# Kernel optimization log

Measured on AMD Instinct MI355X. Metric: run time of the kernel, lower is better.

Reference implementation:

```python
import jax, jax.numpy as jnp
import numpy as np

B, CIN, H, W = 4, 272, 32, 32
D, NHEAD, DFF, E, TOPK, NDEC = 256, 8, 1024, 8, 2, 2
HW = H * W


def _sine_pos():
    npf = D // 2
    ye = jnp.cumsum(jnp.ones((H, W), jnp.float32), 0)
    xe = jnp.cumsum(jnp.ones((H, W), jnp.float32), 1)
    eps, scale = 1e-6, 2.0 * np.pi
    ye = ye / (ye[-1:, :] + eps) * scale
    xe = xe / (xe[:, -1:] + eps) * scale
    t = jnp.arange(npf, dtype=jnp.float32)
    dim_t = 10000.0 ** (2.0 * jnp.floor(t / 2.0) / npf)
    px = xe[:, :, None] / dim_t
    py = ye[:, :, None] / dim_t
    px = jnp.stack((jnp.sin(px[:, :, 0::2]), jnp.cos(px[:, :, 1::2])), axis=3).reshape(H, W, npf)
    py = jnp.stack((jnp.sin(py[:, :, 0::2]), jnp.cos(py[:, :, 1::2])), axis=3).reshape(H, W, npf)
    return jnp.concatenate((py, px), axis=2).reshape(HW, D)


def _ln(v, g, b):
    m = v.mean(-1, keepdims=True)
    var = ((v - m) ** 2).mean(-1, keepdims=True)
    return (v - m) / jnp.sqrt(var + 1e-5) * g + b


def _mha(q_in, k_in, v_in, Wqkv, bqkv, Wo, bo):
    # seq-first [S,B,D], torch nn.MultiheadAttention math (dropout off)
    S = q_in.shape[0]; T = k_in.shape[0]; dh = D // NHEAD
    Wq, Wk, Wv = jnp.split(Wqkv, 3, 0)
    bq, bk, bv = jnp.split(bqkv, 3)
    q = (q_in @ Wq.T + bq).reshape(S, B, NHEAD, dh)
    k = (k_in @ Wk.T + bk).reshape(T, B, NHEAD, dh)
    v = (v_in @ Wv.T + bv).reshape(T, B, NHEAD, dh)
    attn = jax.nn.softmax(jnp.einsum('sbhd,tbhd->bhst', q, k) / np.sqrt(dh), axis=-1)
    o = jnp.einsum('bhst,tbhd->sbhd', attn, v).reshape(S, B, D)
    return o @ Wo.T + bo


def _moe(xt, Wg, bg, W1, b1, W2, b2):
    # FMoETransformerMLP with NaiveGate: top-k gate, per-expert 2-layer MLP, weighted combine
    S = xt.shape[0]
    xf = xt.reshape(-1, D)
    N = xf.shape[0]
    logits = xf @ Wg.T + bg                              # [N, E]
    topv, topi = jax.lax.top_k(logits, TOPK)             # [N, k]
    score = jax.nn.softmax(topv, axis=-1)                # softmax over selected logits
    comb = jnp.zeros((N, E), xf.dtype).at[jnp.arange(N)[:, None], topi].add(score)
    h = jax.nn.relu(jnp.einsum('nd,edh->neh', xf, W1) + b1)   # [N, E, DFF]
    y = jnp.einsum('neh,ehd->ned', h, W2) + b2                # [N, E, D]
    out = jnp.einsum('ne,ned->nd', comb, y)
    return out.reshape(S, B, D)


def setup_inputs() -> dict:
    key = jax.random.key(0)
    ks = iter(jax.random.split(key, 32))
    g = lambda shp, s=0.02: s * jax.random.normal(next(ks), shp, jnp.float32)
    inp = {
        'x': jax.random.normal(next(ks), (B, CIN, H, W), jnp.float32),
        'Wi': g((D, CIN)), 'bi': jnp.zeros((D,), jnp.float32),
        'learned_embed': g((HW, D), 1.0),
        'Wqkv_s': g((3 * D, D)), 'bqkv_s': jnp.zeros((3 * D,), jnp.float32),
        'Wo_s': g((D, D)), 'bo_s': jnp.zeros((D,), jnp.float32),
        'Wqkv_c': g((3 * D, D)), 'bqkv_c': jnp.zeros((3 * D,), jnp.float32),
        'Wo_c': g((D, D)), 'bo_c': jnp.zeros((D,), jnp.float32),
        'ln_g': jnp.ones((4 * NDEC, D), jnp.float32), 'ln_b': jnp.zeros((4 * NDEC, D), jnp.float32),
        'gate_w1': g((E, D)), 'gate_b1': jnp.zeros((E,), jnp.float32),
        'W1a': g((E, D, DFF)), 'b1a': jnp.zeros((E, DFF), jnp.float32),
        'W2a': g((E, DFF, D)), 'b2a': jnp.zeros((E, D), jnp.float32),
        'gate_w2': g((E, D)), 'gate_b2': jnp.zeros((E,), jnp.float32),
        'W1b': g((E, D, DFF)), 'b1b': jnp.zeros((E, DFF), jnp.float32),
        'W2b': g((E, DFF, D)), 'b2b': jnp.zeros((E, D), jnp.float32),
        'Wout': g((CIN, D)), 'bout': jnp.zeros((CIN,), jnp.float32),
    }
    return inp


def reference(x, Wi, bi, learned_embed, Wqkv_s, bqkv_s, Wo_s, bo_s,
              Wqkv_c, bqkv_c, Wo_c, bo_c, ln_g, ln_b,
              gate_w1, gate_b1, W1a, b1a, W2a, b2a,
              gate_w2, gate_b2, W1b, b1b, W2b, b2b, Wout, bout):
    tokens = x.transpose(2, 3, 0, 1).reshape(HW, B, CIN)   # 'b c h w -> (h w) b c'
    src = tokens @ Wi.T + bi                               # input_proj
    pos = _sine_pos()[:, None, :]                          # [HW,1,D] broadcast over batch
    enc = src
    dec = src
    for i in range(NDEC):
        tgt = jnp.broadcast_to(learned_embed[:, None, :], (HW, B, D))
        t2 = _mha(tgt + pos, enc + pos, enc, Wqkv_s, bqkv_s, Wo_s, bo_s)
        tgt = _ln(tgt + t2, ln_g[4 * i], ln_b[4 * i])
        t2 = _mha(tgt + pos, dec + pos, dec, Wqkv_c, bqkv_c, Wo_c, bo_c)
        tgt = _ln(tgt + t2, ln_g[4 * i + 1], ln_b[4 * i + 1])
        od = tgt + _moe(tgt, gate_w1, gate_b1, W1a, b1a, W2a, b2a)   # post-lnorm: residual only
        od = _ln(od, ln_g[4 * i + 2], ln_b[4 * i + 2])
        od = od + _moe(od, gate_w2, gate_b2, W1b, b1b, W2b, b2b)
        dec = _ln(od, ln_g[4 * i + 3], ln_b[4 * i + 3])
    rec = dec @ Wout.T + bout                              # output_proj, [HW,B,CIN]
    feature_rec = rec.reshape(H, W, B, CIN).transpose(2, 3, 0, 1)
    return feature_rec
```

## Files before the change

### kernel.cpp

```cpp
#include <hip/hip_runtime.h>

#define NHW 1024
#define NB 4
#define DM 256
#define NTOK 4096
#define NCIN 272
#define NDFF 1024

typedef unsigned short u16;
typedef unsigned int u32;
typedef __attribute__((ext_vector_type(8))) short s16x8;
typedef __attribute__((ext_vector_type(4))) float f32x4;

static const int GEMM_SMEM32 = (32+32+64+64)*56*2;
static const int GEMM_SMEM64 = (32+32+64+64)*72*2;

__device__ __forceinline__ float4 ld4(const float* p){ return *(const float4*)p; }
__device__ __forceinline__ void st4(float* p, float4 v){ *(float4*)p = v; }

__device__ __forceinline__ void splitf(float x, u16& h, u16& l){
  u32 u = __float_as_uint(x);
  u32 hu = (u + (0x7FFFu + ((u >> 16) & 1u))) >> 16;
  h = (u16)hu;
  float hf = __uint_as_float(hu << 16);
  float r = x - hf;
  u32 v = __float_as_uint(r);
  v += 0x7FFFu + ((v >> 16) & 1u);
  l = (u16)(v >> 16);
}

__device__ __forceinline__ u32 packf(float x){
  u16 h,l; splitf(x,h,l);
  return (u32)h | ((u32)l << 16);
}

__global__ void pos_kernel(float* __restrict__ pos){
  int s = blockIdx.x, d = threadIdx.x;
  int row = s >> 5, col = s & 31;
  float base = (d < 128) ? (float)(row + 1) : (float)(col + 1);
  float val = base / (32.0f + 1e-6f) * 6.2831853071795864f;
  int dd = (d < 128) ? d : d - 128;
  int mf = dd >> 1;
  float f = powf(10000.0f, (float)mf * (1.0f/64.0f));
  float a = val / f;
  pos[s*DM + d] = (dd & 1) ? cosf(a) : sinf(a);
}

__global__ void tin_kernel(const float* __restrict__ x, float* __restrict__ tok){
  int idx = blockIdx.x*256 + threadIdx.x;
  if (idx >= NTOK*NCIN) return;
  int c = idx % NCIN;
  int n = idx / NCIN;
  int s = n >> 2, b = n & 3;
  tok[idx] = x[((long)(b*NCIN + c))*NHW + s];
}
__global__ void tout_kernel(const float* __restrict__ rec, float* __restrict__ out){
  int idx = blockIdx.x*256 + threadIdx.x;
  if (idx >= NTOK*NCIN) return;
  int s = idx & (NHW-1);
  int bc = idx >> 10;
  int b = bc / NCIN, c = bc % NCIN;
  out[idx] = rec[((long)(s*NB + b))*NCIN + c];
}

__global__ __launch_bounds__(256) void tconv_kernel(const float* __restrict__ in,
    u16* __restrict__ oh, u16* __restrict__ ol, int K, int N){
  __shared__ float tile[32][33];
  long base = (long)blockIdx.z * (long)K * (long)N;
  int k0 = blockIdx.y*32, n0 = blockIdx.x*32;
  int tx = threadIdx.x & 31, ty = threadIdx.x >> 5;
  #pragma unroll
  for (int i=0;i<32;i+=8)
    tile[ty+i][tx] = in[base + (long)(k0+ty+i)*N + n0+tx];
  __syncthreads();
  #pragma unroll
  for (int i=0;i<32;i+=8){
    float v = tile[tx][ty+i];
    u16 h,l; splitf(v,h,l);
    long o = base + (long)(n0+ty+i)*K + k0+tx;
    oh[o]=h; ol[o]=l;
  }
}

__global__ void wsplit_kernel(const float* __restrict__ in, u16* __restrict__ oh,
    u16* __restrict__ ol, int n){
  int i = blockIdx.x*256 + threadIdx.x;
  if (i < n){ u16 h,l; splitf(in[i],h,l); oh[i]=h; ol[i]=l; }
}

template<bool GROUPED, bool INDIRECT, int ASRC, bool RELU, int CDST, int BK>
__device__ __forceinline__ void sgemm_body(
    const void* __restrict__ Av, int lda,
    const float* __restrict__ pos,
    const u16* __restrict__ Bhp, const u16* __restrict__ Blp, int ldb,
    const float* __restrict__ bias,
    void* __restrict__ Cv, int ldc,
    int M, int N, int K,
    const int* __restrict__ map,
    const int* __restrict__ cnt,
    const int* __restrict__ offs,
    const int* __restrict__ jmap,
    const float* __restrict__ sflat,
    long strideB, int strideBias, int e)
{
  constexpr int BM = 32;
  constexpr int NSEG = BK/32;
  constexpr int SW = (BK==32) ? 56 : 72;
  int rows = GROUPED ? cnt[e] : M;
  int bn = blockIdx.x, bm = blockIdx.y;
  if (bm*BM >= rows) return;
  int row0 = GROUPED ? offs[e] : 0;
  const float* Af = (const float*)Av;
  const u32*   Ap = (const u32*)Av;
  if (GROUPED){ Bhp += (long)e*strideB; Blp += (long)e*strideB; }
  const float* biasp = bias ? (GROUPED ? bias + (long)e*strideBias : bias) : nullptr;

  extern __shared__ u16 smem[];
  u16* Ah = smem;
  u16* Al = Ah + BM*SW;
  u16* Bh = Al + BM*SW;
  u16* Bl = Bh + 64*SW;

  int tid = threadIdx.x;
  int w = tid >> 6, ln = tid & 63;
  int wm = w >> 1, wn = w & 1;
  int lr = ln & 15, lh = ln >> 4;
  int srow = tid >> 2, sseg = tid & 3;

  int bgrow = bn*64 + srow;
  bool bok = bgrow < N;
  int agrow = bm*BM + srow;
  bool aok = (tid < BM*4) && (agrow < rows);
  long arow = 0;
  if (aok) arow = INDIRECT ? (long)map[row0 + agrow] : (long)(row0 + agrow);

  const f32x4 z4 = {0.f,0.f,0.f,0.f};
  f32x4 acc0 = z4, acc1 = z4;
  const s16x8 z8 = {0,0,0,0,0,0,0,0};

  s16x8 rBh[NSEG], rBl[NSEG];
  uint4 rA0[NSEG], rA1[NSEG];
  float4 rP0[NSEG], rP1[NSEG];
  float rinv[NSEG];

  auto load_stage = [&](int k0){
    #pragma unroll
    for (int s=0; s<NSEG; s++){
      int kk = k0 + s*32 + sseg*8;
      bool kok = kk < K;
      rBh[s] = z8; rBl[s] = z8;
      if (bok && kok){
        rBh[s] = *(const s16x8*)&Bhp[(long)bgrow*ldb + kk];
        rBl[s] = *(const s16x8*)&Blp[(long)bgrow*ldb + kk];
      }
      if (tid < BM*4){
        rA0[s] = make_uint4(0,0,0,0); rA1[s] = make_uint4(0,0,0,0);
        if (ASRC==2 || ASRC==3 || ASRC==5){
          rP0[s] = make_float4(0.f,0.f,0.f,0.f); rP1[s] = rP0[s]; rinv[s] = 0.f;
        }
        if (aok && kok){
          if (ASRC == 1){
            rA0[s] = *(const uint4*)&Ap[arow*lda + kk];
            rA1[s] = *(const uint4*)&Ap[arow*lda + kk + 4];
          } else if (ASRC == 5){
            long aoff = arow*(long)lda + kk;
            rA0[s] = *(const uint4*)&Af[aoff];
            rA1[s] = *(const uint4*)&Af[aoff + 4];
            rP0[s] = ld4(&Af[(long)NTOK*DM + aoff]);
            rP1[s] = ld4(&Af[(long)NTOK*DM + aoff + 4]);
            int h = kk >> 5;
            float l0 = pos[arow*8 + h];
            float l1 = pos[65536 + arow*8 + h];
            rinv[s] = 1.f / (l0 + l1);
          } else {
            long aoff = (ASRC==3 ? (long)(arow>>2) : arow)*lda + kk;
            rA0[s] = *(const uint4*)&Af[aoff];
            rA1[s] = *(const uint4*)&Af[aoff + 4];
            if (ASRC==2 || ASRC==3){
              long poff = (long)(arow>>2)*DM + kk;
              rP0[s] = ld4(&pos[poff]);
              rP1[s] = ld4(&pos[poff + 4]);
            }
          }
        }
      }
    }
  };

  auto write_stage = [&](){
    #pragma unroll
    for (int s=0; s<NSEG; s++){
      *(s16x8*)&Bh[srow*SW + s*32 + sseg*8] = rBh[s];
      *(s16x8*)&Bl[srow*SW + s*32 + sseg*8] = rBl[s];
      if (tid < BM*4){
        s16x8 hv, lv;
        if (ASRC == 1){
          u32 ws[8] = {rA0[s].x,rA0[s].y,rA0[s].z,rA0[s].w,rA1[s].x,rA1[s].y,rA1[s].z,rA1[s].w};
          #pragma unroll
          for (int t=0;t<8;t++){ hv[t]=(short)(ws[t]&0xFFFFu); lv[t]=(short)(ws[t]>>16); }
        } else {
          float xs[8] = {__uint_as_float(rA0[s].x),__uint_as_float(rA0[s].y),
                         __uint_as_float(rA0[s].z),__uint_as_float(rA0[s].w),
                         __uint_as_float(rA1[s].x),__uint_as_float(rA1[s].y),
                         __uint_as_float(rA1[s].z),__uint_as_float(rA1[s].w)};
          if (ASRC==2 || ASRC==3){
            xs[0]+=rP0[s].x; xs[1]+=rP0[s].y; xs[2]+=rP0[s].z; xs[3]+=rP0[s].w;
            xs[4]+=rP1[s].x; xs[5]+=rP1[s].y; xs[6]+=rP1[s].z; xs[7]+=rP1[s].w;
          }
          if (ASRC==5){
            float iv = rinv[s];
            xs[0]=(xs[0]+rP0[s].x)*iv; xs[1]=(xs[1]+rP0[s].y)*iv;
            xs[2]=(xs[2]+rP0[s].z)*iv; xs[3]=(xs[3]+rP0[s].w)*iv;
            xs[4]=(xs[4]+rP1[s].x)*iv; xs[5]=(xs[5]+rP1[s].y)*iv;
            xs[6]=(xs[6]+rP1[s].z)*iv; xs[7]=(xs[7]+rP1[s].w)*iv;
          }
          #pragma unroll
          for (int t=0;t<8;t++){ u16 hh,ll; splitf(xs[t],hh,ll); hv[t]=(short)hh; lv[t]=(short)ll; }
        }
        *(s16x8*)&Ah[srow*SW + s*32 + sseg*8] = hv;
        *(s16x8*)&Al[srow*SW + s*32 + sseg*8] = lv;
      }
    }
  };

  load_stage(0);
  for (int k0 = 0; k0 < K; k0 += BK){
    write_stage();
    __syncthreads();
    if (k0 + BK < K) load_stage(k0 + BK);
    #pragma unroll
    for (int s=0; s<NSEG; s++){
      int co = s*32 + lh*8;
      s16x8 a0h = *(const s16x8*)&Ah[(wm*16 + lr)*SW + co];
      s16x8 a0l = *(const s16x8*)&Al[(wm*16 + lr)*SW + co];
      s16x8 b0h = *(const s16x8*)&Bh[(wn*32      + lr)*SW + co];
      s16x8 b1h = *(const s16x8*)&Bh[(wn*32 + 16 + lr)*SW + co];
      s16x8 b0l = *(const s16x8*)&Bl[(wn*32      + lr)*SW + co];
      s16x8 b1l = *(const s16x8*)&Bl[(wn*32 + 16 + lr)*SW + co];
      acc0 = __builtin_amdgcn_mfma_f32_16x16x32_bf16(a0h, b0h, acc0, 0,0,0);
      acc1 = __builtin_amdgcn_mfma_f32_16x16x32_bf16(a0h, b1h, acc1, 0,0,0);
      acc0 = __builtin_amdgcn_mfma_f32_16x16x32_bf16(a0h, b0l, acc0, 0,0,0);
      acc1 = __builtin_amdgcn_mfma_f32_16x16x32_bf16(a0h, b1l, acc1, 0,0,0);
      acc0 = __builtin_amdgcn_mfma_f32_16x16x32_bf16(a0l, b0h, acc0, 0,0,0);
      acc1 = __builtin_amdgcn_mfma_f32_16x16x32_bf16(a0l, b1h, acc1, 0,0,0);
    }
    __syncthreads();
  }

  int c0 = bn*64 + wn*32 + lr;
  int c1 = c0 + 16;
  float bv0 = (biasp && c0 < N) ? biasp[c0] : 0.f;
  float bv1 = (biasp && c1 < N) ? biasp[c1] : 0.f;
  int rbase = bm*BM + wm*16 + lh*4;
  auto stc = [&](int gr, int gc, float vv){
    if (gr < rows && gc < N){
      float t = RELU ? fmaxf(vv, 0.f) : vv;
      if (CDST == 1){
        ((u32*)Cv)[(long)(row0+gr)*ldc + gc] = packf(t);
      } else if (CDST == 2){
        int ts = jmap[row0+gr];
        ((float*)Cv)[(long)ts*ldc + gc] = t * sflat[ts];
      } else {
        ((float*)Cv)[(long)(row0+gr)*ldc + gc] = t;
      }
    }
  };
  #pragma unroll
  for (int r = 0; r < 4; r++){
    stc(rbase + r, c0, acc0[r] + bv0);
    stc(rbase + r, c1, acc1[r] + bv1);
  }
}

__global__ __launch_bounds__(256) void gemm_in(const float* A, const u16* Bh_, const u16* Bl_,
    const float* bias, float* C){
  sgemm_body<false,false,0,false,0,32>(A, NCIN, nullptr, Bh_, Bl_, NCIN, bias, C, DM,
      NTOK, DM, NCIN, nullptr, nullptr, nullptr, nullptr, nullptr, 0, 0, 0);
}

__global__ __launch_bounds__(256) void gemm_out_k(const float* A, const u16* Bh_, const u16* Bl_,
    const float* bias, float* C){
  sgemm_body<false,false,0,false,0,32>(A, DM, nullptr, Bh_, Bl_, DM, bias, C, NCIN,
      NTOK, NCIN, DM, nullptr, nullptr, nullptr, nullptr, nullptr, 0, 0, 0);
}

__global__ __launch_bounds__(256) void gemm_wos(const float* OpB, const float* lB,
    const u16* Bh_, const u16* Bl_, const float* bias, float* C){
  sgemm_body<false,false,5,false,0,32>(OpB, DM, lB, Bh_, Bl_, DM, bias, C, DM,
      NTOK, DM, DM, nullptr, nullptr, nullptr, nullptr, nullptr, 0, 0, 0);
}

__global__ __launch_bounds__(256) void gemm_woc(const float* OpB, const float* lB,
    const u16* Bh_, const u16* Bl_, const float* bias, float* C){
  sgemm_body<false,false,5,false,0,32>(OpB, DM, lB, Bh_, Bl_, DM, bias, C, DM,
      NTOK, DM, DM, nullptr, nullptr, nullptr, nullptr, nullptr, 0, 0, 0);
}

template<int MQ, int MK>
__device__ __forceinline__ void qkv_body(const float* Aq, const float* Ak, const float* Avv,
    const float* pos, const u16* Bwh, const u16* Bwl, const float* bias,
    u32* Cq, u32* Ck, u32* Cvv){
  int z = blockIdx.z;
  const float* A = z==0 ? Aq : (z==1 ? Ak : Avv);
  u32* C = z==0 ? Cq : (z==1 ? Ck : Cvv);
  const u16* Bph = Bwh + (long)z*256*DM;
  const u16* Bpl = Bwl + (long)z*256*DM;
  const float* bp = bias + z*256;
  int mode = z==0 ? MQ : (z==1 ? MK : 0);
  if (mode == 3)
    sgemm_body<false,false,3,false,1,32>(A, DM, pos, Bph, Bpl, DM, bp, C, DM,
        NTOK, DM, DM, nullptr, nullptr, nullptr, nullptr, nullptr, 0, 0, 0);
  else if (mode == 2)
    sgemm_body<false,false,2,false,1,32>(A, DM, pos, Bph, Bpl, DM, bp, C, DM,
        NTOK, DM, DM, nullptr, nullptr, nullptr, nullptr, nullptr, 0, 0, 0);
  else
    sgemm_body<false,false,0,false,1,32>(A, DM, pos, Bph, Bpl, DM, bp, C, DM,
        NTOK, DM, DM, nullptr, nullptr, nullptr, nullptr, nullptr, 0, 0, 0);
}

__global__ __launch_bounds__(256) void gemm_qkv_s(const float* Aq, const float* Ak,
    const float* Avv, const float* pos, const u16* Bwh, const u16* Bwl, const float* bias,
    u32* Cq, u32* Ck, u32* Cvv){
  qkv_body<3,2>(Aq, Ak, Avv, pos, Bwh, Bwl, bias, Cq, Ck, Cvv);
}
__global__ __launch_bounds__(256) void gemm_qkv_c(const float* Aq, const float* Ak,
    const float* Avv, const float* pos, const u16* Bwh, const u16* Bwl, const float* bias,
    u32* Cq, u32* Ck, u32* Cvv){
  qkv_body<2,2>(Aq, Ak, Avv, pos, Bwh, Bwl, bias, Cq, Ck, Cvv);
}

__global__ __launch_bounds__(256) void gemm_m1(const float* A, const u16* Bh_, const u16* Bl_,
    const float* bias, u32* C, const int* map, const int* cnt, const int* offs){
  sgemm_body<true,true,0,true,1,32>(A, DM, nullptr, Bh_, Bl_, DM, bias, C, NDFF,
      0, NDFF, DM, map, cnt, offs, nullptr, nullptr, 262144L, NDFF, blockIdx.z);
}

__global__ __launch_bounds__(256) void gemm_m2(const u32* A, const u16* Bh_, const u16* Bl_,
    const float* bias, float* C, const int* cnt, const int* offs,
    const int* jmap, const float* sflat){
  sgemm_body<true,false,1,false,2,64>(A, NDFF, nullptr, Bh_, Bl_, NDFF, bias, C, DM,
      0, DM, NDFF, nullptr, cnt, offs, jmap, sflat, 262144L, DM, blockIdx.z);
}

__global__ __launch_bounds__(256) void attn_mfma(const u32* __restrict__ Q,
    const u32* __restrict__ Kb, const u32* __restrict__ Vb,
    float* __restrict__ OpBase, float* __restrict__ lBase)
{
  __shared__ u16 Kh[64*40], Kl[64*40];
  __shared__ u16 Vh[32*72], Vl[32*72];
  __shared__ u16 Ph[4][16*72], Pl[4][16*72];

  int qt = blockIdx.x, bh = blockIdx.y, z = blockIdx.z;
  int b = bh >> 3, h = bh & 7;
  int tid = threadIdx.x;
  int wv = tid >> 6, ln = tid & 63;
  int lr = ln & 15, lh = ln >> 4;
  const float scale = 0.17677669529663687f;
  int kt0 = z*8, kt1 = z*8 + 8;
  float* Op   = OpBase + (long)z*NTOK*DM;
  float* lArr = lBase + (long)z*65536;

  s16x8 qh, ql;
  {
    long qrow = ((long)((qt*64 + wv*16 + lr)*NB + b))*DM + h*32 + lh*8;
    uint4 p0 = *(const uint4*)&Q[qrow];
    uint4 p1 = *(const uint4*)&Q[qrow + 4];
    u32 ws[8] = {p0.x,p0.y,p0.z,p0.w,p1.x,p1.y,p1.z,p1.w};
    #pragma unroll
    for (int t=0;t<8;t++){ qh[t]=(short)(ws[t]&0xFFFFu); ql[t]=(short)(ws[t]>>16); }
  }

  int skey = tid >> 2, soct = tid & 3;
  int vkey0 = tid >> 3,        vd0 = (tid & 7) << 2;
  int vkey1 = (tid + 256) >> 3, vd1 = ((tid + 256) & 7) << 2;

  uint4 rK0, rK1, rV0, rV1;

  auto load_kv = [&](int kt){
    long gk = ((long)((kt*64 + skey)*NB + b))*DM + h*32 + soct*8;
    rK0 = *(const uint4*)&Kb[gk];
    rK1 = *(const uint4*)&Kb[gk + 4];
    rV0 = *(const uint4*)&Vb[((long)((kt*64 + vkey0)*NB + b))*DM + h*32 + vd0];
    rV1 = *(const uint4*)&Vb[((long)((kt*64 + vkey1)*NB + b))*DM + h*32 + vd1];
  };

  auto write_kv = [&](){
    u32 ws[8] = {rK0.x,rK0.y,rK0.z,rK0.w,rK1.x,rK1.y,rK1.z,rK1.w};
    s16x8 hv, lv;
    #pragma unroll
    for (int t=0;t<8;t++){ hv[t]=(short)(ws[t]&0xFFFFu); lv[t]=(short)(ws[t]>>16); }
    *(s16x8*)&Kh[skey*40 + soct*8] = hv;
    *(s16x8*)&Kl[skey*40 + soct*8] = lv;
    u32 v0[4] = {rV0.x,rV0.y,rV0.z,rV0.w};
    u32 v1[4] = {rV1.x,rV1.y,rV1.z,rV1.w};
    #pragma unroll
    for (int t=0;t<4;t++){
      Vh[(vd0+t)*72 + vkey0] = (u16)(v0[t]&0xFFFFu);
      Vl[(vd0+t)*72 + vkey0] = (u16)(v0[t]>>16);
      Vh[(vd1+t)*72 + vkey1] = (u16)(v1[t]&0xFFFFu);
      Vl[(vd1+t)*72 + vkey1] = (u16)(v1[t]>>16);
    }
  };

  const f32x4 z4 = {0.f,0.f,0.f,0.f};
  f32x4 oacc0 = z4, oacc1 = z4;
  float lp[4] = {0.f,0.f,0.f,0.f};

  load_kv(kt0);
  for (int kt = kt0; kt < kt1; kt++){
    write_kv();
    __syncthreads();
    if (kt + 1 < kt1) load_kv(kt + 1);

    #pragma unroll
    for (int s16t=0; s16t<4; s16t++){
      s16x8 kbh = *(const s16x8*)&Kh[(s16t*16 + lr)*40 + lh*8];
      s16x8 kbl = *(const s16x8*)&Kl[(s16t*16 + lr)*40 + lh*8];
      f32x4 a = z4;
      a = __builtin_amdgcn_mfma_f32_16x16x32_bf16(qh, kbh, a, 0,0,0);
      a = __builtin_amdgcn_mfma_f32_16x16x32_bf16(qh, kbl, a, 0,0,0);
      a = __builtin_amdgcn_mfma_f32_16x16x32_bf16(ql, kbh, a, 0,0,0);
      #pragma unroll
      for (int r=0;r<4;r++){
        float p = __expf(a[r]*scale);
        lp[r] += p;
        u16 hh,ll; splitf(p,hh,ll);
        int off = (lh*4 + r)*72 + s16t*16 + lr;
        Ph[wv][off] = hh;
        Pl[wv][off] = ll;
      }
    }
    #pragma unroll
    for (int ks=0; ks<2; ks++){
      s16x8 pah = *(const s16x8*)&Ph[wv][lr*72 + ks*32 + lh*8];
      s16x8 pal = *(const s16x8*)&Pl[wv][lr*72 + ks*32 + lh*8];
      s16x8 vh0 = *(const s16x8*)&Vh[lr*72      + ks*32 + lh*8];
      s16x8 vl0 = *(const s16x8*)&Vl[lr*72      + ks*32 + lh*8];
      s16x8 vh1 = *(const s16x8*)&Vh[(16+lr)*72 + ks*32 + lh*8];
      s16x8 vl1 = *(const s16x8*)&Vl[(16+lr)*72 + ks*32 + lh*8];
      oacc0 = __builtin_amdgcn_mfma_f32_16x16x32_bf16(pah, vh0, oacc0, 0,0,0);
      oacc0 = __builtin_amdgcn_mfma_f32_16x16x32_bf16(pah, vl0, oacc0, 0,0,0);
      oacc0 = __builtin_amdgcn_mfma_f32_16x16x32_bf16(pal, vh0, oacc0, 0,0,0);
      oacc1 = __builtin_amdgcn_mfma_f32_16x16x32_bf16(pah, vh1, oacc1, 0,0,0);
      oacc1 = __builtin_amdgcn_mfma_f32_16x16x32_bf16(pah, vl1, oacc1, 0,0,0);
      oacc1 = __builtin_amdgcn_mfma_f32_16x16x32_bf16(pal, vh1, oacc1, 0,0,0);
    }
    __syncthreads();
  }
  #pragma unroll
  for (int mask=1; mask<=8; mask<<=1){
    #pragma unroll
    for (int r=0;r<4;r++) lp[r] += __shfl_xor(lp[r], mask);
  }
  #pragma unroll
  for (int r=0;r<4;r++){
    int q = qt*64 + wv*16 + lh*4 + r;
    long n = (long)q*NB + b;
    long orow = n*DM + h*32;
    Op[orow + lr]      = oacc0[r];
    Op[orow + 16 + lr] = oacc1[r];
    if (lr == 0) lArr[n*8 + h] = lp[r];
  }
}

__device__ __forceinline__ float wave_sum(float v){
  #pragma unroll
  for (int m=1; m<64; m<<=1) v += __shfl_xor(v, m);
  return v;
}

__device__ __forceinline__ float4 ln_finish(float4 a, const float* g, const float* beta, int lane){
  float sum = wave_sum(a.x+a.y+a.z+a.w);
  float sq  = wave_sum(a.x*a.x + a.y*a.y + a.z*a.z + a.w*a.w);
  float mean = sum * (1.f/DM);
  float var  = sq * (1.f/DM) - mean*mean;
  float inv = 1.0f / sqrtf(var + 1e-5f);
  float4 gg = ld4(&g[lane*4]);
  float4 bb = ld4(&beta[lane*4]);
  float4 ov;
  ov.x = (a.x-mean)*inv*gg.x + bb.x;
  ov.y = (a.y-mean)*inv*gg.y + bb.y;
  ov.z = (a.z-mean)*inv*gg.z + bb.z;
  ov.w = (a.w-mean)*inv*gg.w + bb.w;
  return ov;
}

__device__ __forceinline__ void gate_from_regs(float4 ov, int row, int lane,
    const float* GW, const float* GB, float* scores, int* topi){
  float lg[8];
  #pragma unroll
  for (int e=0; e<8; e++){
    float4 wv = ld4(&GW[e*DM + lane*4]);
    lg[e] = ov.x*wv.x + ov.y*wv.y + ov.z*wv.z + ov.w*wv.w;
  }
  #pragma unroll
  for (int mask=1; mask<64; mask<<=1){
    #pragma unroll
    for (int e=0; e<8; e++) lg[e] += __shfl_xor(lg[e], mask);
  }
  #pragma unroll
  for (int e=0; e<8; e++) lg[e] += GB[e];
  int i0 = 0; float v0 = lg[0];
  #pragma unroll
  for (int e=1; e<8; e++) if (lg[e] > v0){ v0 = lg[e]; i0 = e; }
  int i1 = -1; float v1 = -1e30f;
  #pragma unroll
  for (int e=0; e<8; e++) if (e != i0 && lg[e] > v1){ v1 = lg[e]; i1 = e; }
  if (lane == 0){
    float ee = expf(v1 - v0);
    float inv = 1.f/(1.f + ee);
    scores[row*2]   = inv;
    scores[row*2+1] = ee*inv;
    topi[row*2]   = i0;
    topi[row*2+1] = i1;
  }
}

__global__ __launch_bounds__(256) void add_ln_le(const float* __restrict__ A,
    const float* __restrict__ Bv, const float* __restrict__ g, const float* __restrict__ beta,
    float* __restrict__ out)
{
  int row = blockIdx.x*4 + (threadIdx.x >> 6);
  int lane = threadIdx.x & 63;
  float4 a = ld4(&A[(long)(row>>2)*DM + lane*4]);
  float4 b = ld4(&Bv[(long)row*DM + lane*4]);
  a.x+=b.x; a.y+=b.y; a.z+=b.z; a.w+=b.w;
  float4 ov = ln_finish(a, g, beta, lane);
  st4(&out[(long)row*DM + lane*4], ov);
}

__global__ __launch_bounds__(256) void add_ln_gate(const float* __restrict__ A,
    const float* __restrict__ Bv, const float* __restrict__ g, const float* __restrict__ beta,
    float* __restrict__ out, const float* __restrict__ GW, const float* __restrict__ GB,
    float* __restrict__ scores, int* __restrict__ topi)
{
  int row = blockIdx.x*4 + (threadIdx.x >> 6);
  int lane = threadIdx.x & 63;
  float4 a = ld4(&A[(long)row*DM + lane*4]);
  float4 b = ld4(&Bv[(long)row*DM + lane*4]);
  a.x+=b.x; a.y+=b.y; a.z+=b.z; a.w+=b.w;
  float4 ov = ln_finish(a, g, beta, lane);
  st4(&out[(long)row*DM + lane*4], ov);
  gate_from_regs(ov, row, lane, GW, GB, scores, topi);
}

__global__ __launch_bounds__(256) void moe_ln_gate_k(const float* __restrict__ base,
    const float* __restrict__ yt,
    const float* __restrict__ g, const float* __restrict__ beta, float* __restrict__ out,
    const float* __restrict__ GW, const float* __restrict__ GB,
    float* __restrict__ scores2, int* __restrict__ topi2)
{
  int row = blockIdx.x*4 + (threadIdx.x >> 6);
  int lane = threadIdx.x & 63;
  float4 a  = ld4(&base[(long)row*DM + lane*4]);
  float4 y0 = ld4(&yt[(long)(row*2)*DM + lane*4]);
  float4 y1 = ld4(&yt[(long)(row*2+1)*DM + lane*4]);
  a.x += y0.x + y1.x;
  a.y += y0.y + y1.y;
  a.z += y0.z + y1.z;
  a.w += y0.w + y1.w;
  float4 ov = ln_finish(a, g, beta, lane);
  st4(&out[(long)row*DM + lane*4], ov);
  gate_from_regs(ov, row, lane, GW, GB, scores2, topi2);
}

__global__ __launch_bounds__(256) void moe_ln_fin_k(const float* __restrict__ base,
    const float* __restrict__ yt,
    const float* __restrict__ g, const float* __restrict__ beta, float* __restrict__ out)
{
  int row = blockIdx.x*4 + (threadIdx.x >> 6);
  int lane = threadIdx.x & 63;
  float4 a  = ld4(&base[(long)row*DM + lane*4]);
  float4 y0 = ld4(&yt[(long)(row*2)*DM + lane*4]);
  float4 y1 = ld4(&yt[(long)(row*2+1)*DM + lane*4]);
  a.x += y0.x + y1.x;
  a.y += y0.y + y1.y;
  a.z += y0.z + y1.z;
  a.w += y0.w + y1.w;
  float4 ov = ln_finish(a, g, beta, lane);
  st4(&out[(long)row*DM + lane*4], ov);
}

__global__ void offs_assign(const int* __restrict__ topi, int* __restrict__ cnt_g,
    int* __restrict__ offs_g, int* __restrict__ map, int* __restrict__ jmap)
{
  __shared__ int hist[72];
  __shared__ int offs[8];
  __shared__ int c2[8];
  int tid = threadIdx.x;
  if (tid < 72) hist[tid] = 0;
  __syncthreads();
  for (int idx = tid; idx < 2*NTOK; idx += 256){
    int e = topi[idx];
    atomicAdd(&hist[e*9 + (tid & 7)], 1);
  }
  __syncthreads();
  if (tid == 0){
    int o = 0;
    #pragma unroll
    for (int e=0; e<8; e++){
      int c = 0;
      #pragma unroll
      for (int s=0; s<8; s++) c += hist[e*9 + s];
      cnt_g[e] = c;
      offs[e] = o;
      offs_g[e] = o;
      o += c;
      c2[e] = 0;
    }
  }
  __syncthreads();
  for (int n = tid; n < NTOK; n += 256){
    #pragma unroll
    for (int j=0; j<2; j++){
      int e = topi[n*2+j];
      int slot = atomicAdd(&c2[e], 1);
      int r = offs[e] + slot;
      map[r] = n;
      jmap[r] = n*2 + j;
    }
  }
}

extern "C" void kernel_launch(void* const* d_in, const int* in_sizes, int n_in,
                              void* d_out, int out_size, void* d_ws, size_t ws_size,
                              hipStream_t stream)
{
  const float* x      = (const float*)d_in[0];
  const float* Wi     = (const float*)d_in[1];
  const float* bi     = (const float*)d_in[2];
  const float* le     = (const float*)d_in[3];
  const float* Wqkv_s = (const float*)d_in[4];
  const float* bqkv_s = (const float*)d_in[5];
  const float* Wo_s   = (const float*)d_in[6];
  const float* bo_s   = (const float*)d_in[7];
  const float* Wqkv_c = (const float*)d_in[8];
  const float* bqkv_c = (const float*)d_in[9];
  const float* Wo_c   = (const float*)d_in[10];
  const float* bo_c   = (const float*)d_in[11];
  const float* ln_g   = (const float*)d_in[12];
  const float* ln_b   = (const float*)d_in[13];
  const float* gw1    = (const float*)d_in[14];
  const float* gb1    = (const float*)d_in[15];
  const float* W1a    = (const float*)d_in[16];
  const float* b1a    = (const float*)d_in[17];
  const float* W2a    = (const float*)d_in[18];
  const float* b2a    = (const float*)d_in[19];
  const float* gw2    = (const float*)d_in[20];
  const float* gb2    = (const float*)d_in[21];
  const float* W1b    = (const float*)d_in[22];
  const float* b1b    = (const float*)d_in[23];
  const float* W2b    = (const float*)d_in[24];
  const float* b2b    = (const float*)d_in[25];
  const float* Wout   = (const float*)d_in[26];
  const float* bout   = (const float*)d_in[27];

  float* w = (float*)d_ws;
  const long SZ = 1048576;
  float* pos  = w;
  float* src  = pos  + 262144;
  float* t2s  = src  + SZ;
  float* tgtA = t2s  + SZ;
  float* dec  = tgtA + SZ;
  float* od   = dec;
  float* od2  = dec  + SZ;
  float* yt   = od2  + SZ;
  float* scoresA = yt + 2097152;
  float* scoresB = scoresA + 8192;
  u16* wsp  = (u16*)(scoresB + 8192);
  u16* W1ah = wsp;             u16* W1al = wsp + 2097152;
  u16* W1bh = wsp + 4194304;   u16* W1bl = wsp + 6291456;
  u16* W2ah = wsp + 8388608;   u16* W2al = wsp + 10485760;
  u16* W2bh = wsp + 12582912;  u16* W2bl = wsp + 14680064;
  u16* dwp  = wsp + 16777216;
  u16* Wih   = dwp;            u16* Wil   = dwp + 69632;
  u16* Wqsh  = dwp + 139264;   u16* Wqsl  = dwp + 335872;
  u16* Wosh  = dwp + 532480;   u16* Wosl  = dwp + 598016;
  u16* Wqch  = dwp + 663552;   u16* Wqcl  = dwp + 860160;
  u16* Woch  = dwp + 1056768;  u16* Wocl  = dwp + 1122304;
  u16* Wouth = dwp + 1187840;  u16* Woutl = dwp + 1257472;
  float* R   = (float*)(dwp + 1327104);
  float* tok = R;
  u32*  q    = (u32*)R;
  u32*  k    = (u32*)(R + SZ);
  u32*  v    = (u32*)(R + 2*SZ);
  float* OpB = R + 4*SZ;
  float* lB  = R + 6*SZ;
  u32*  hg   = (u32*)R;
  float* rec = R;
  int* ip    = (int*)(R + 8388608);
  int* topiA = ip;
  int* topiB = ip + 8192;
  int* map   = ip + 16384;
  int* jmapA = ip + 24576;
  int* jmapB = ip + 32768;
  int* cnts  = ip + 40960;
  int* offsg = ip + 40992;

  dim3 blk(256);
  dim3 gDense(4, 128, 1);
  dim3 gQKV(4, 128, 3);
  dim3 gMoe1(16, 128, 8);
  dim3 gMoe2(4, 128, 8);
  dim3 gAttn(16, 32, 2);

  pos_kernel<<<NHW, DM, 0, stream>>>(pos);
  tin_kernel<<<(NTOK*NCIN + 255)/256, blk, 0, stream>>>(x, tok);

  tconv_kernel<<<dim3(32, 8, 8), blk, 0, stream>>>(W1a, W1ah, W1al, DM,   NDFF);
  tconv_kernel<<<dim3(32, 8, 8), blk, 0, stream>>>(W1b, W1bh, W1bl, DM,   NDFF);
  tconv_kernel<<<dim3(8, 32, 8), blk, 0, stream>>>(W2a, W2ah, W2al, NDFF, DM);
  tconv_kernel<<<dim3(8, 32, 8), blk, 0, stream>>>(W2b, W2bh, W2bl, NDFF, DM);
  wsplit_kernel<<<272, blk, 0, stream>>>(Wi,     Wih,   Wil,   69632);
  wsplit_kernel<<<768, blk, 0, stream>>>(Wqkv_s, Wqsh,  Wqsl,  196608);
  wsplit_kernel<<<256, blk, 0, stream>>>(Wo_s,   Wosh,  Wosl,  65536);
  wsplit_kernel<<<768, blk, 0, stream>>>(Wqkv_c, Wqch,  Wqcl,  196608);
  wsplit_kernel<<<256, blk, 0, stream>>>(Wo_c,   Woch,  Wocl,  65536);
  wsplit_kernel<<<272, blk, 0, stream>>>(Wout,   Wouth, Woutl, 69632);

  gemm_in<<<gDense, blk, GEMM_SMEM32, stream>>>(tok, Wih, Wil, bi, src);

  gemm_qkv_s<<<gQKV, blk, GEMM_SMEM32, stream>>>(le, src, src, pos, Wqsh, Wqsl, bqkv_s, q, k, v);
  attn_mfma<<<gAttn, blk, 0, stream>>>(q, k, v, OpB, lB);
  gemm_wos<<<gDense, blk, GEMM_SMEM32, stream>>>(OpB, lB, Wosh, Wosl, bo_s, t2s);

  const float* decIn = src;
  for (int i = 0; i < 2; i++){
    int* cntA = cnts + (i*2)*8;   int* offsA = offsg + (i*2)*8;
    int* cntB = cnts + (i*2+1)*8; int* offsB = offsg + (i*2+1)*8;

    add_ln_le<<<1024, blk, 0, stream>>>(le, t2s, ln_g + (4*i)*DM, ln_b + (4*i)*DM, tgtA);
    gemm_qkv_c<<<gQKV, blk, GEMM_SMEM32, stream>>>(tgtA, decIn, decIn, pos, Wqch, Wqcl, bqkv_c, q, k, v);
    attn_mfma<<<gAttn, blk, 0, stream>>>(q, k, v, OpB, lB);
    gemm_woc<<<gDense, blk, GEMM_SMEM32, stream>>>(OpB, lB, Woch, Wocl, bo_c, (float*)k);
    add_ln_gate<<<1024, blk, 0, stream>>>(tgtA, (float*)k, ln_g + (4*i+1)*DM, ln_b + (4*i+1)*DM, od,
        gw1, gb1, scoresA, topiA);

    offs_assign<<<1, blk, 0, stream>>>(topiA, cntA, offsA, map, jmapA);
    gemm_m1<<<gMoe1, blk, GEMM_SMEM32, stream>>>(od, W1ah, W1al, b1a, hg, map, cntA, offsA);
    gemm_m2<<<gMoe2, blk, GEMM_SMEM64, stream>>>(hg, W2ah, W2al, b2a, yt, cntA, offsA,
        jmapA, scoresA);
    moe_ln_gate_k<<<1024, blk, 0, stream>>>(od, yt,
        ln_g + (4*i+2)*DM, ln_b + (4*i+2)*DM, od2, gw2, gb2, scoresB, topiB);

    offs_assign<<<1, blk, 0, stream>>>(topiB, cntB, offsB, map, jmapB);
    gemm_m1<<<gMoe1, blk, GEMM_SMEM32, stream>>>(od2, W1bh, W1bl, b1b, hg, map, cntB, offsB);
    gemm_m2<<<gMoe2, blk, GEMM_SMEM64, stream>>>(hg, W2bh, W2bl, b2b, yt, cntB, offsB,
        jmapB, scoresB);
    moe_ln_fin_k<<<1024, blk, 0, stream>>>(od2, yt,
        ln_g + (4*i+3)*DM, ln_b + (4*i+3)*DM, dec);

    decIn = dec;
  }

  gemm_out_k<<<dim3(5,128,1), blk, GEMM_SMEM32, stream>>>(dec, Wouth, Woutl, bout, rec);
  tout_kernel<<<(NTOK*NCIN + 255)/256, blk, 0, stream>>>(rec, (float*)d_out);
}
```

Baseline: 616.7 us.

## Double-buffer GEMM register prefetch two K-tiles ahead

Replaces the single register staging set in the split-bf16 GEMM with two alternating sets, so global loads are issued two K-tiles ahead of use. This gives the loads more time to complete before the results are written to shared memory, hiding global latency behind more MFMA work. The cost is roughly doubled staging registers, which may lower occupancy or cause spills. Out-of-range tiles rely on the existing kk<K guard.

```diff
diff --git a/kernel.cpp b/kernel.cpp
--- a/kernel.cpp
+++ b/kernel.cpp
@@ -138,12 +138,16 @@
   f32x4 acc0 = z4, acc1 = z4;
   const s16x8 z8 = {0,0,0,0,0,0,0,0};
 
-  s16x8 rBh[NSEG], rBl[NSEG];
-  uint4 rA0[NSEG], rA1[NSEG];
-  float4 rP0[NSEG], rP1[NSEG];
-  float rinv[NSEG];
-
-  auto load_stage = [&](int k0){
+  s16x8 rBh0[NSEG], rBl0[NSEG], rBh1[NSEG], rBl1[NSEG];
+  uint4 rA00[NSEG], rA10[NSEG], rA01[NSEG], rA11[NSEG];
+  float4 rP00[NSEG], rP10[NSEG], rP01[NSEG], rP11[NSEG];
+  float rinv0[NSEG], rinv1[NSEG];
+
+  auto load_st = [&](s16x8 (&rBh)[NSEG], s16x8 (&rBl)[NSEG],
+                     uint4 (&rA0)[NSEG], uint4 (&rA1)[NSEG],
+                     float4 (&rP0)[NSEG], float4 (&rP1)[NSEG],
+                     float (&rinv)[NSEG], int t){
+    int k0 = t*BK;
     #pragma unroll
     for (int s=0; s<NSEG; s++){
       int kk = k0 + s*32 + sseg*8;
@@ -187,7 +191,10 @@
     }
   };
 
-  auto write_stage = [&](){
+  auto write_st = [&](s16x8 (&rBh)[NSEG], s16x8 (&rBl)[NSEG],
+                      uint4 (&rA0)[NSEG], uint4 (&rA1)[NSEG],
+                      float4 (&rP0)[NSEG], float4 (&rP1)[NSEG],
+                      float (&rinv)[NSEG]){
     #pragma unroll
     for (int s=0; s<NSEG; s++){
       *(s16x8*)&Bh[srow*SW + s*32 + sseg*8] = rBh[s];
@@ -223,11 +230,7 @@
     }
   };
 
-  load_stage(0);
-  for (int k0 = 0; k0 < K; k0 += BK){
-    write_stage();
-    __syncthreads();
-    if (k0 + BK < K) load_stage(k0 + BK);
+  auto compute_tile = [&](){
     #pragma unroll
     for (int s=0; s<NSEG; s++){
       int co = s*32 + lh*8;
@@ -244,7 +247,24 @@
       acc0 = __builtin_amdgcn_mfma_f32_16x16x32_bf16(a0l, b0h, acc0, 0,0,0);
       acc1 = __builtin_amdgcn_mfma_f32_16x16x32_bf16(a0l, b1h, acc1, 0,0,0);
     }
+  };
+
+  const int NT = (K + BK - 1) / BK;
+  load_st(rBh0,rBl0,rA00,rA10,rP00,rP10,rinv0, 0);
+  load_st(rBh1,rBl1,rA01,rA11,rP01,rP11,rinv1, 1);
+  for (int t = 0; t < NT; t += 2){
+    write_st(rBh0,rBl0,rA00,rA10,rP00,rP10,rinv0);
     __syncthreads();
+    load_st(rBh0,rBl0,rA00,rA10,rP00,rP10,rinv0, t+2);
+    compute_tile();
+    __syncthreads();
+    if (t+1 < NT){
+      write_st(rBh1,rBl1,rA01,rA11,rP01,rP11,rinv1);
+      __syncthreads();
+      load_st(rBh1,rBl1,rA01,rA11,rP01,rP11,rinv1, t+3);
+      compute_tile();
+      __syncthreads();
+    }
   }
 
   int c0 = bn*64 + wn*32 + lr;
```

Result: slower. 646.2 us (+4.8%).
